# Kernel optimization log

Measured on AMD Instinct MI355X. Metric: run time of the kernel, lower is better.

The kernel has to match this reference:

```python
import jax, jax.numpy as jnp
import numpy as np

N = 100000
E = 1600000
F_IN = 128
F_HID = 128


def gcn_conv(x, src, dst, deg_inv_sqrt, W, b, n_nodes):
    # x: [N, Fin] -> [N, Fout]; symmetric-normalized aggregation with self-loops
    h = x @ W  # [N, Fout]
    norm = deg_inv_sqrt[src] * deg_inv_sqrt[dst]  # [E+N] (self-loops appended)
    msgs = h[src] * norm[:, None]  # [E+N, Fout]
    out = jax.ops.segment_sum(msgs, dst, num_segments=n_nodes)
    return out + b


def setup_inputs() -> dict:
    key = jax.random.key(0)
    k = jax.random.split(key, 8)
    x = jax.random.normal(k[0], (N, F_IN), dtype=jnp.float32)
    edge_index = jax.random.randint(k[1], (2, E), 0, N, dtype=jnp.int32)
    s = 1.0 / np.sqrt(F_IN)
    W1 = jax.random.uniform(k[2], (F_IN, F_HID), jnp.float32, -s, s)
    b1 = jnp.zeros((F_HID,), jnp.float32)
    s2 = 1.0 / np.sqrt(F_HID)
    W2 = jax.random.uniform(k[3], (F_HID, F_HID), jnp.float32, -s2, s2)
    b2 = jnp.zeros((F_HID,), jnp.float32)
    W3 = jax.random.uniform(k[4], (F_HID, 1), jnp.float32, -s2, s2)
    b3 = jnp.zeros((1,), jnp.float32)
    return {"x": x, "edge_index": edge_index, "W1": W1, "b1": b1,
            "W2": W2, "b2": b2, "W3": W3, "b3": b3}


def reference(x, edge_index, W1, b1, W2, b2, W3, b3):
    n = x.shape[0]
    loops = jnp.arange(n, dtype=edge_index.dtype)
    src = jnp.concatenate([edge_index[0], loops])  # add self-loops
    dst = jnp.concatenate([edge_index[1], loops])
    deg = jax.ops.segment_sum(jnp.ones_like(dst, dtype=x.dtype), dst, num_segments=n)
    deg_inv_sqrt = jnp.where(deg > 0, jax.lax.rsqrt(deg), 0.0)

    h = gcn_conv(x, src, dst, deg_inv_sqrt, W1, b1, n)
    h = jax.nn.relu(h)  # dropout is identity at inference
    h = gcn_conv(h, src, dst, deg_inv_sqrt, W2, b2, n)
    h = jax.nn.relu(h)
    h = gcn_conv(h, src, dst, deg_inv_sqrt, W3, b3, n)
    return jax.nn.sigmoid(h)  # [N, 1]
```

## Files before the change

kernel.cpp:

```cpp
#include <hip/hip_runtime.h>
#include <cstdint>
#include <cstddef>

#define NN 100000
#define NE 1600000
#define FD 128
#define NXCD 8
#define RNODES ((NN + NXCD - 1) / NXCD)

__global__ void k_hist(const int* __restrict__ dst, int* __restrict__ cnt, int e) {
    int i = blockIdx.x * blockDim.x + threadIdx.x;
    if (i < e) atomicAdd(&cnt[dst[i]], 1);
}

__global__ __launch_bounds__(1024) void k_scan1(const int* __restrict__ cnt,
                                                int* __restrict__ excl,
                                                int* __restrict__ bsum, int n) {
    __shared__ int sh[1024];
    int i = blockIdx.x * 1024 + threadIdx.x;
    int v = (i < n) ? cnt[i] : 0;
    sh[threadIdx.x] = v;
    __syncthreads();
    for (int off = 1; off < 1024; off <<= 1) {
        int t = (threadIdx.x >= off) ? sh[threadIdx.x - off] : 0;
        __syncthreads();
        sh[threadIdx.x] += t;
        __syncthreads();
    }
    if (i < n) excl[i] = sh[threadIdx.x] - v;
    if (threadIdx.x == 1023) bsum[blockIdx.x] = sh[1023];
}

__global__ void k_scan2(int* __restrict__ bsum, int nb) {
    __shared__ int sh[128];
    int t = threadIdx.x;
    int v = (t < nb) ? bsum[t] : 0;
    sh[t] = v;
    __syncthreads();
    for (int off = 1; off < 128; off <<= 1) {
        int u = (t >= off) ? sh[t - off] : 0;
        __syncthreads();
        sh[t] += u;
        __syncthreads();
    }
    if (t < nb) bsum[t] = sh[t] - v;
}

__global__ void k_scan3(int* __restrict__ excl, const int* __restrict__ bsum,
                        int* __restrict__ cursor, const int* __restrict__ cnt,
                        float* __restrict__ dis, int n, int e) {
    int i = blockIdx.x * blockDim.x + threadIdx.x;
    if (i < n) {
        int v = excl[i] + bsum[i >> 10];
        excl[i] = v;
        cursor[i] = v;
        dis[i] = rsqrtf((float)(cnt[i] + 1));
    }
    if (i == 0) excl[n] = e;
}

__global__ __launch_bounds__(256) void k_fill(const int* __restrict__ src,
                                              const int* __restrict__ dst,
                                              int* __restrict__ cursor,
                                              int* __restrict__ col, int e) {
    const int xcd   = blockIdx.x & 7;
    const int chunk = blockIdx.x >> 3;
    const int lo = xcd * RNODES;
    const int hi = lo + RNODES;
    const int base = chunk * 1024 + threadIdx.x * 4;
    if (base >= e) return;
    int4 d4 = *(const int4*)(dst + base);
    #pragma unroll
    for (int j = 0; j < 4; ++j) {
        int d = (&d4.x)[j];
        if (d >= lo && d < hi) {
            int s   = src[base + j];
            int pos = atomicAdd(&cursor[d], 1);
            col[pos] = s;
        }
    }
}

__global__ __launch_bounds__(256) void k_gemm(const float* __restrict__ X,
                                              const float* __restrict__ W,
                                              float* __restrict__ H, int n) {
    __shared__ float At[64][68];
    __shared__ float Ws[64][64];
    const int t  = threadIdx.x;
    const int tx = t & 15;
    const int ty = t >> 4;
    const int rb = blockIdx.x * 64;
    const int cb = blockIdx.y * 64;

    float acc[4][4] = {};

    for (int c = 0; c < 2; ++c) {
        #pragma unroll
        for (int r = 0; r < 4; ++r) {
            int f   = t + 256 * r;
            int row = f >> 4;
            int kc  = (f & 15) << 2;
            float4 v = make_float4(0.f, 0.f, 0.f, 0.f);
            int grow = rb + row;
            if (grow < n)
                v = *(const float4*)(X + (size_t)grow * FD + c * 64 + kc);
            At[kc + 0][row] = v.x;
            At[kc + 1][row] = v.y;
            At[kc + 2][row] = v.z;
            At[kc + 3][row] = v.w;
            *(float4*)&Ws[row][kc] =
                *(const float4*)(W + (size_t)(c * 64 + row) * FD + cb + kc);
        }
        __syncthreads();
        #pragma unroll 8
        for (int k = 0; k < 64; ++k) {
            float4 a = *(const float4*)&At[k][ty * 4];
            float4 b = *(const float4*)&Ws[k][tx * 4];
            acc[0][0] = fmaf(a.x, b.x, acc[0][0]);
            acc[0][1] = fmaf(a.x, b.y, acc[0][1]);
            acc[0][2] = fmaf(a.x, b.z, acc[0][2]);
            acc[0][3] = fmaf(a.x, b.w, acc[0][3]);
            acc[1][0] = fmaf(a.y, b.x, acc[1][0]);
            acc[1][1] = fmaf(a.y, b.y, acc[1][1]);
            acc[1][2] = fmaf(a.y, b.z, acc[1][2]);
            acc[1][3] = fmaf(a.y, b.w, acc[1][3]);
            acc[2][0] = fmaf(a.z, b.x, acc[2][0]);
            acc[2][1] = fmaf(a.z, b.y, acc[2][1]);
            acc[2][2] = fmaf(a.z, b.z, acc[2][2]);
            acc[2][3] = fmaf(a.z, b.w, acc[2][3]);
            acc[3][0] = fmaf(a.w, b.x, acc[3][0]);
            acc[3][1] = fmaf(a.w, b.y, acc[3][1]);
            acc[3][2] = fmaf(a.w, b.z, acc[3][2]);
            acc[3][3] = fmaf(a.w, b.w, acc[3][3]);
        }
        __syncthreads();
    }

    #pragma unroll
    for (int i = 0; i < 4; ++i) {
        int grow = rb + ty * 4 + i;
        if (grow < n)
            *(float4*)(H + (size_t)grow * FD + cb + tx * 4) =
                make_float4(acc[i][0], acc[i][1], acc[i][2], acc[i][3]);
    }
}

__global__ __launch_bounds__(256) void k_agg(const float* __restrict__ h,
                                             const float* __restrict__ dis,
                                             const int* __restrict__ rp,
                                             const int* __restrict__ col,
                                             const float* __restrict__ bias,
                                             float* __restrict__ out, int n) {
    int i    = (int)((blockIdx.x * (size_t)blockDim.x + threadIdx.x) >> 6);
    int lane = threadIdx.x & 63;
    if (i >= n) return;
    float di = dis[i];
    float2 acc = ((const float2*)(h + (size_t)i * FD))[lane];
    float w0 = di * di;
    acc.x *= w0; acc.y *= w0;
    const int e0 = rp[i], e1 = rp[i + 1];
    for (int base = e0; base < e1; base += 64) {
        int m = e1 - base; if (m > 64) m = 64;
        int s = 0; float w = 0.f;
        if (lane < m) { s = col[base + lane]; w = dis[s] * di; }
        int j = 0;
        for (; j + 8 <= m; j += 8) {
            int ss[8]; float ww[8]; float2 vv[8];
            #pragma unroll
            for (int q = 0; q < 8; ++q) { ss[q] = __shfl(s, j + q); ww[q] = __shfl(w, j + q); }
            #pragma unroll
            for (int q = 0; q < 8; ++q)
                vv[q] = ((const float2*)(h + (size_t)ss[q] * FD))[lane];
            #pragma unroll
            for (int q = 0; q < 8; ++q) {
                acc.x = fmaf(ww[q], vv[q].x, acc.x);
                acc.y = fmaf(ww[q], vv[q].y, acc.y);
            }
        }
        for (; j < m; ++j) {
            int sj = __shfl(s, j); float wj = __shfl(w, j);
            float2 v = ((const float2*)(h + (size_t)sj * FD))[lane];
            acc.x = fmaf(wj, v.x, acc.x);
            acc.y = fmaf(wj, v.y, acc.y);
        }
    }
    float2 b = ((const float2*)bias)[lane];
    acc.x = fmaxf(acc.x + b.x, 0.f);
    acc.y = fmaxf(acc.y + b.y, 0.f);
    ((float2*)(out + (size_t)i * FD))[lane] = acc;
}

__global__ __launch_bounds__(256) void k_agg_mv(const float* __restrict__ h,
                                                const float* __restrict__ dis,
                                                const int* __restrict__ rp,
                                                const int* __restrict__ col,
                                                const float* __restrict__ bias,
                                                const float* __restrict__ W3,
                                                float* __restrict__ h3, int n) {
    int i    = (int)((blockIdx.x * (size_t)blockDim.x + threadIdx.x) >> 6);
    int lane = threadIdx.x & 63;
    if (i >= n) return;
    float di = dis[i];
    float2 acc = ((const float2*)(h + (size_t)i * FD))[lane];
    float w0 = di * di;
    acc.x *= w0; acc.y *= w0;
    const int e0 = rp[i], e1 = rp[i + 1];
    for (int base = e0; base < e1; base += 64) {
        int m = e1 - base; if (m > 64) m = 64;
        int s = 0; float w = 0.f;
        if (lane < m) { s = col[base + lane]; w = dis[s] * di; }
        int j = 0;
        for (; j + 8 <= m; j += 8) {
            int ss[8]; float ww[8]; float2 vv[8];
            #pragma unroll
            for (int q = 0; q < 8; ++q) { ss[q] = __shfl(s, j + q); ww[q] = __shfl(w, j + q); }
            #pragma unroll
            for (int q = 0; q < 8; ++q)
                vv[q] = ((const float2*)(h + (size_t)ss[q] * FD))[lane];
            #pragma unroll
            for (int q = 0; q < 8; ++q) {
                acc.x = fmaf(ww[q], vv[q].x, acc.x);
                acc.y = fmaf(ww[q], vv[q].y, acc.y);
            }
        }
        for (; j < m; ++j) {
            int sj = __shfl(s, j); float wj = __shfl(w, j);
            float2 v = ((const float2*)(h + (size_t)sj * FD))[lane];
            acc.x = fmaf(wj, v.x, acc.x);
            acc.y = fmaf(wj, v.y, acc.y);
        }
    }
    float2 b = ((const float2*)bias)[lane];
    acc.x = fmaxf(acc.x + b.x, 0.f);
    acc.y = fmaxf(acc.y + b.y, 0.f);
    float2 w3 = ((const float2*)W3)[lane];
    float sdot = acc.x * w3.x + acc.y * w3.y;
    #pragma unroll
    for (int off = 32; off; off >>= 1) sdot += __shfl_xor(sdot, off);
    if (lane == 0) h3[i] = sdot;
}

__global__ __launch_bounds__(256) void k_agg1(const float* __restrict__ h3,
                                              const float* __restrict__ dis,
                                              const int* __restrict__ rp,
                                              const int* __restrict__ col,
                                              const float* __restrict__ b3,
                                              float* __restrict__ out, int n) {
    int i    = (int)((blockIdx.x * (size_t)blockDim.x + threadIdx.x) >> 6);
    int lane = threadIdx.x & 63;
    if (i >= n) return;
    float di  = dis[i];
    float acc = (lane == 0) ? di * di * h3[i] : 0.f;
    const int e0 = rp[i], e1 = rp[i + 1];
    for (int base = e0 + lane; base < e1; base += 64) {
        int s = col[base];
        acc = fmaf(dis[s] * di, h3[s], acc);
    }
    #pragma unroll
    for (int off = 32; off; off >>= 1) acc += __shfl_xor(acc, off);
    if (lane == 0) {
        float v = acc + b3[0];
        out[i] = 1.f / (1.f + expf(-v));
    }
}

static inline size_t alg(size_t x) { return (x + 255) & ~(size_t)255; }

extern "C" void kernel_launch(void* const* d_in, const int* in_sizes, int n_in,
                              void* d_out, int out_size, void* d_ws, size_t ws_size,
                              hipStream_t stream) {
    const float* x   = (const float*)d_in[0];
    const int*   ei  = (const int*)d_in[1];
    const float* W1  = (const float*)d_in[2];
    const float* b1  = (const float*)d_in[3];
    const float* W2  = (const float*)d_in[4];
    const float* b2  = (const float*)d_in[5];
    const float* W3  = (const float*)d_in[6];
    const float* b3  = (const float*)d_in[7];
    float*       out = (float*)d_out;

    const int n = NN, e = NE;
    const int* src = ei;
    const int* dst = ei + e;

    char* w = (char*)d_ws;
    float* dis    = (float*)w;  w += alg((size_t)n * 4);
    int*   cnt    = (int*)w;    w += alg((size_t)n * 4);
    int*   rp     = (int*)w;    w += alg((size_t)(n + 1) * 4);
    int*   cursor = (int*)w;    w += alg((size_t)n * 4);
    int*   bsum   = (int*)w;    w += alg((size_t)128 * 4);
    int*   col    = (int*)w;    w += alg((size_t)e * 4);
    float* bufA   = (float*)w;  w += alg((size_t)n * FD * 4);
    float* bufB   = (float*)w;  w += alg((size_t)n * FD * 4);
    float* h3     = (float*)w;  w += alg((size_t)n * 4);

    hipMemsetAsync(cnt, 0, (size_t)n * 4, stream);

    const int B = 256;
    const int gE = (e + B - 1) / B;
    const int gN = (n + B - 1) / B;
    const int nScan = (n + 1023) / 1024;

    k_hist<<<gE, B, 0, stream>>>(dst, cnt, e);
    k_scan1<<<nScan, 1024, 0, stream>>>(cnt, rp, bsum, n);
    k_scan2<<<1, 128, 0, stream>>>(bsum, nScan);
    k_scan3<<<gN, B, 0, stream>>>(rp, bsum, cursor, cnt, dis, n, e);

    const int nChunk = (e + 1023) / 1024;
    k_fill<<<nChunk * NXCD, B, 0, stream>>>(src, dst, cursor, col, e);

    dim3 gGemm((n + 63) / 64, 2);
    const int gWave = (n * 64 + B - 1) / B;

    k_gemm<<<gGemm, B, 0, stream>>>(x, W1, bufA, n);
    k_agg<<<gWave, B, 0, stream>>>(bufA, dis, rp, col, b1, bufB, n);
    k_gemm<<<gGemm, B, 0, stream>>>(bufB, W2, bufA, n);
    k_agg_mv<<<gWave, B, 0, stream>>>(bufA, dis, rp, col, b2, W3, h3, n);
    k_agg1<<<gWave, B, 0, stream>>>(h3, dis, rp, col, b3, out, n);
}
```

Baseline: 597.2 us.

## Precompute edge weights in CSR fill and prefetch wave-uniform edge indices in aggregation

```diff
diff --git a/kernel.cpp b/kernel.cpp
--- a/kernel.cpp
+++ b/kernel.cpp
@@ -8,9 +8,20 @@
 #define NXCD 8
 #define RNODES ((NN + NXCD - 1) / NXCD)
 
-__global__ void k_hist(const int* __restrict__ dst, int* __restrict__ cnt, int e) {
-    int i = blockIdx.x * blockDim.x + threadIdx.x;
-    if (i < e) atomicAdd(&cnt[dst[i]], 1);
+__global__ __launch_bounds__(256) void k_hist(const int* __restrict__ dst,
+                                              int* __restrict__ cnt, int e) {
+    const int xcd   = blockIdx.x & 7;
+    const int chunk = blockIdx.x >> 3;
+    const int lo = xcd * RNODES;
+    const int hi = lo + RNODES;
+    const int base = chunk * 1024 + threadIdx.x * 4;
+    if (base >= e) return;
+    int4 d4 = *(const int4*)(dst + base);
+    #pragma unroll
+    for (int j = 0; j < 4; ++j) {
+        int d = (&d4.x)[j];
+        if (d >= lo && d < hi) atomicAdd(&cnt[d], 1);
+    }
 }
 
 __global__ __launch_bounds__(1024) void k_scan1(const int* __restrict__ cnt,
@@ -62,7 +73,9 @@
 __global__ __launch_bounds__(256) void k_fill(const int* __restrict__ src,
                                               const int* __restrict__ dst,
                                               int* __restrict__ cursor,
-                                              int* __restrict__ col, int e) {
+                                              int* __restrict__ col,
+                                              float* __restrict__ wedge,
+                                              const float* __restrict__ dis, int e) {
     const int xcd   = blockIdx.x & 7;
     const int chunk = blockIdx.x >> 3;
     const int lo = xcd * RNODES;
@@ -76,7 +89,8 @@
         if (d >= lo && d < hi) {
             int s   = src[base + j];
             int pos = atomicAdd(&cursor[d], 1);
-            col[pos] = s;
+            col[pos]   = s;
+            wedge[pos] = dis[s] * dis[d];
         }
     }
 }
@@ -145,105 +159,78 @@
     }
 }
 
+template <int MODE>
 __global__ __launch_bounds__(256) void k_agg(const float* __restrict__ h,
                                              const float* __restrict__ dis,
                                              const int* __restrict__ rp,
                                              const int* __restrict__ col,
+                                             const float* __restrict__ wedge,
                                              const float* __restrict__ bias,
+                                             const float* __restrict__ W3,
                                              float* __restrict__ out, int n) {
-    int i    = (int)((blockIdx.x * (size_t)blockDim.x + threadIdx.x) >> 6);
+    int wid  = (int)((blockIdx.x * (size_t)blockDim.x + threadIdx.x) >> 6);
     int lane = threadIdx.x & 63;
+    int i = __builtin_amdgcn_readfirstlane(wid);
     if (i >= n) return;
     float di = dis[i];
     float2 acc = ((const float2*)(h + (size_t)i * FD))[lane];
     float w0 = di * di;
     acc.x *= w0; acc.y *= w0;
     const int e0 = rp[i], e1 = rp[i + 1];
-    for (int base = e0; base < e1; base += 64) {
-        int m = e1 - base; if (m > 64) m = 64;
-        int s = 0; float w = 0.f;
-        if (lane < m) { s = col[base + lane]; w = dis[s] * di; }
-        int j = 0;
-        for (; j + 8 <= m; j += 8) {
-            int ss[8]; float ww[8]; float2 vv[8];
+
+    const int nfull = (e1 - e0) >> 3;
+    int j = e0;
+    int sA[8]; float wA[8];
+    if (nfull > 0) {
+        #pragma unroll
+        for (int q = 0; q < 8; ++q) { sA[q] = col[j + q]; wA[q] = wedge[j + q]; }
+    }
+    for (int g = 0; g < nfull; ++g) {
+        int sB[8]; float wB[8];
+        const int jn = j + 8;
+        if (g + 1 < nfull) {
             #pragma unroll
-            for (int q = 0; q < 8; ++q) { ss[q] = __shfl(s, j + q); ww[q] = __shfl(w, j + q); }
-            #pragma unroll
-            for (int q = 0; q < 8; ++q)
-                vv[q] = ((const float2*)(h + (size_t)ss[q] * FD))[lane];
-            #pragma unroll
-            for (int q = 0; q < 8; ++q) {
-                acc.x = fmaf(ww[q], vv[q].x, acc.x);
-                acc.y = fmaf(ww[q], vv[q].y, acc.y);
-            }
-        }
-        for (; j < m; ++j) {
-            int sj = __shfl(s, j); float wj = __shfl(w, j);
-            float2 v = ((const float2*)(h + (size_t)sj * FD))[lane];
-            acc.x = fmaf(wj, v.x, acc.x);
-            acc.y = fmaf(wj, v.y, acc.y);
-        }
-    }
+            for (int q = 0; q < 8; ++q) { sB[q] = col[jn + q]; wB[q] = wedge[jn + q]; }
+        }
+        float2 vv[8];
+        #pragma unroll
+        for (int q = 0; q < 8; ++q)
+            vv[q] = ((const float2*)(h + (size_t)sA[q] * FD))[lane];
+        #pragma unroll
+        for (int q = 0; q < 8; ++q) {
+            acc.x = fmaf(wA[q], vv[q].x, acc.x);
+            acc.y = fmaf(wA[q], vv[q].y, acc.y);
+        }
+        #pragma unroll
+        for (int q = 0; q < 8; ++q) { sA[q] = sB[q]; wA[q] = wB[q]; }
+        j = jn;
+    }
+    for (; j < e1; ++j) {
+        int s = col[j]; float w = wedge[j];
+        float2 v = ((const float2*)(h + (size_t)s * FD))[lane];
+        acc.x = fmaf(w, v.x, acc.x);
+        acc.y = fmaf(w, v.y, acc.y);
+    }
+
     float2 b = ((const float2*)bias)[lane];
     acc.x = fmaxf(acc.x + b.x, 0.f);
     acc.y = fmaxf(acc.y + b.y, 0.f);
-    ((float2*)(out + (size_t)i * FD))[lane] = acc;
-}
-
-__global__ __launch_bounds__(256) void k_agg_mv(const float* __restrict__ h,
-                                                const float* __restrict__ dis,
-                                                const int* __restrict__ rp,
-                                                const int* __restrict__ col,
-                                                const float* __restrict__ bias,
-                                                const float* __restrict__ W3,
-                                                float* __restrict__ h3, int n) {
-    int i    = (int)((blockIdx.x * (size_t)blockDim.x + threadIdx.x) >> 6);
-    int lane = threadIdx.x & 63;
-    if (i >= n) return;
-    float di = dis[i];
-    float2 acc = ((const float2*)(h + (size_t)i * FD))[lane];
-    float w0 = di * di;
-    acc.x *= w0; acc.y *= w0;
-    const int e0 = rp[i], e1 = rp[i + 1];
-    for (int base = e0; base < e1; base += 64) {
-        int m = e1 - base; if (m > 64) m = 64;
-        int s = 0; float w = 0.f;
-        if (lane < m) { s = col[base + lane]; w = dis[s] * di; }
-        int j = 0;
-        for (; j + 8 <= m; j += 8) {
-            int ss[8]; float ww[8]; float2 vv[8];
-            #pragma unroll
-            for (int q = 0; q < 8; ++q) { ss[q] = __shfl(s, j + q); ww[q] = __shfl(w, j + q); }
-            #pragma unroll
-            for (int q = 0; q < 8; ++q)
-                vv[q] = ((const float2*)(h + (size_t)ss[q] * FD))[lane];
-            #pragma unroll
-            for (int q = 0; q < 8; ++q) {
-                acc.x = fmaf(ww[q], vv[q].x, acc.x);
-                acc.y = fmaf(ww[q], vv[q].y, acc.y);
-            }
-        }
-        for (; j < m; ++j) {
-            int sj = __shfl(s, j); float wj = __shfl(w, j);
-            float2 v = ((const float2*)(h + (size_t)sj * FD))[lane];
-            acc.x = fmaf(wj, v.x, acc.x);
-            acc.y = fmaf(wj, v.y, acc.y);
-        }
-    }
-    float2 b = ((const float2*)bias)[lane];
-    acc.x = fmaxf(acc.x + b.x, 0.f);
-    acc.y = fmaxf(acc.y + b.y, 0.f);
-    float2 w3 = ((const float2*)W3)[lane];
-    float sdot = acc.x * w3.x + acc.y * w3.y;
-    #pragma unroll
-    for (int off = 32; off; off >>= 1) sdot += __shfl_xor(sdot, off);
-    if (lane == 0) h3[i] = sdot;
+    if (MODE == 0) {
+        ((float2*)(out + (size_t)i * FD))[lane] = acc;
+    } else {
+        float2 w3 = ((const float2*)W3)[lane];
+        float sdot = acc.x * w3.x + acc.y * w3.y;
+        #pragma unroll
+        for (int off = 32; off; off >>= 1) sdot += __shfl_xor(sdot, off);
+        if (lane == 0) out[i] = sdot;
+    }
 }
 
 __global__ __launch_bounds__(256) void k_agg1(const float* __restrict__ h3,
                                               const float* __restrict__ dis,
                                               const int* __restrict__ rp,
                                               const int* __restrict__ col,
+                                              const float* __restrict__ wedge,
                                               const float* __restrict__ b3,
                                               float* __restrict__ out, int n) {
     int i    = (int)((blockIdx.x * (size_t)blockDim.x + threadIdx.x) >> 6);
@@ -253,8 +240,7 @@
     float acc = (lane == 0) ? di * di * h3[i] : 0.f;
     const int e0 = rp[i], e1 = rp[i + 1];
     for (int base = e0 + lane; base < e1; base += 64) {
-        int s = col[base];
-        acc = fmaf(dis[s] * di, h3[s], acc);
+        acc = fmaf(wedge[base], h3[col[base]], acc);
     }
     #pragma unroll
     for (int off = 32; off; off >>= 1) acc += __shfl_xor(acc, off);
@@ -290,6 +276,7 @@
     int*   cursor = (int*)w;    w += alg((size_t)n * 4);
     int*   bsum   = (int*)w;    w += alg((size_t)128 * 4);
     int*   col    = (int*)w;    w += alg((size_t)e * 4);
+    float* wedge  = (float*)w;  w += alg((size_t)e * 4);
     float* bufA   = (float*)w;  w += alg((size_t)n * FD * 4);
     float* bufB   = (float*)w;  w += alg((size_t)n * FD * 4);
     float* h3     = (float*)w;  w += alg((size_t)n * 4);
@@ -297,24 +284,22 @@
     hipMemsetAsync(cnt, 0, (size_t)n * 4, stream);
 
     const int B = 256;
-    const int gE = (e + B - 1) / B;
     const int gN = (n + B - 1) / B;
     const int nScan = (n + 1023) / 1024;
-
-    k_hist<<<gE, B, 0, stream>>>(dst, cnt, e);
+    const int nChunk = (e + 1023) / 1024;
+
+    k_hist<<<nChunk * NXCD, B, 0, stream>>>(dst, cnt, e);
     k_scan1<<<nScan, 1024, 0, stream>>>(cnt, rp, bsum, n);
     k_scan2<<<1, 128, 0, stream>>>(bsum, nScan);
     k_scan3<<<gN, B, 0, stream>>>(rp, bsum, cursor, cnt, dis, n, e);
-
-    const int nChunk = (e + 1023) / 1024;
-    k_fill<<<nChunk * NXCD, B, 0, stream>>>(src, dst, cursor, col, e);
+    k_fill<<<nChunk * NXCD, B, 0, stream>>>(src, dst, cursor, col, wedge, dis, e);
 
     dim3 gGemm((n + 63) / 64, 2);
     const int gWave = (n * 64 + B - 1) / B;
 
     k_gemm<<<gGemm, B, 0, stream>>>(x, W1, bufA, n);
-    k_agg<<<gWave, B, 0, stream>>>(bufA, dis, rp, col, b1, bufB, n);
+    k_agg<0><<<gWave, B, 0, stream>>>(bufA, dis, rp, col, wedge, b1, W3, bufB, n);
     k_gemm<<<gGemm, B, 0, stream>>>(bufB, W2, bufA, n);
-    k_agg_mv<<<gWave, B, 0, stream>>>(bufA, dis, rp, col, b2, W3, h3, n);
-    k_agg1<<<gWave, B, 0, stream>>>(h3, dis, rp, col, b3, out, n);
-}
+    k_agg<1><<<gWave, B, 0, stream>>>(bufA, dis, rp, col, wedge, b2, W3, h3, n);
+    k_agg1<<<gWave, B, 0, stream>>>(h3, dis, rp, col, wedge, b3, out, n);
+}
```

Result: no change. 593.6 us (-0.6%).
